# Kernel tuning notes

Measured on AMD Instinct MI355X. Metric: run time of the kernel, lower is better.

## Reference

```python
import jax, jax.numpy as jnp
from jax import lax
import numpy as np

ALIGN = 6                 # AlignW: pad width up to a multiple of align_width=6
W_BITS = 5
A_BITS = 5
A_MASK = (1 << A_BITS) - 1  # direct_conv2d bit-packs activations: keep low A_bits
DN = ('NCHW', 'OIHW', 'NCHW')


def _align_w(a):
    pad = (-a.shape[-1]) % ALIGN
    if pad:
        a = jnp.pad(a, ((0, 0), (0, 0), (0, 0), (0, pad)))
    return a


def _conv_relu(a, w, b):
    # nn.Conv2d(kernel_size=3, padding=2) + ReLU
    y = lax.conv_general_dilated(a, w, (1, 1), [(2, 2), (2, 2)], dimension_numbers=DN)
    return jax.nn.relu(y + b[None, :, None, None])


def _dc_conv(a, w):
    # DC_layer: integer direct conv2d, W_bits-quantized weights, A_bits activations,
    # stride 1, no padding (valid).
    aq = jnp.bitwise_and(a, A_MASK)
    return lax.conv_general_dilated(aq, w, (1, 1), [(0, 0), (0, 0)], dimension_numbers=DN,
                                    preferred_element_type=jnp.int32)


def _maxpool2(a):
    if jnp.issubdtype(a.dtype, jnp.floating):
        init = np.float32(-np.inf)
    else:
        init = np.int32(np.iinfo(np.int32).min)
    return lax.reduce_window(a, init, lax.max, (1, 1, 2, 2), (1, 1, 2, 2), 'VALID')


def _forward(x, ws, bs, qs, fc_w, fc_b):
    a = x
    k = 0
    for n in (2, 2, 3):          # float VGG blocks: [64,64,M, 128,128,M, 256,256,256,M]
        for _ in range(n):
            a = _conv_relu(_align_w(a), ws[k], bs[k])
            k += 1
        a = _maxpool2(a)
    # dequant stub is identity; x.int() truncates toward zero (a >= 0 after ReLU)
    xi = lax.stop_gradient(a).astype(jnp.int32)
    k = 0
    for n in (3, 3):             # DC blocks: [512,512,512,M, 512,512,512,M]
        for _ in range(n):
            xi = _dc_conv(_align_w(xi), qs[k])
            k += 1
        xi = _maxpool2(xi)
    # classifier: AdaptiveAvgPool2d((1,1)) + Flatten + Linear(512, 1000)
    pooled = jnp.mean(xi.astype(jnp.float32), axis=(2, 3))
    return pooled @ fc_w.T + fc_b


def setup_inputs() -> dict:
    key = jax.random.key(0)
    ks = jax.random.split(key, 24)
    d = {}
    d['x'] = jax.random.uniform(ks[0], (16, 3, 224, 224), jnp.float32) * 8.0
    conv_cfg = [(3, 64), (64, 64), (64, 128), (128, 128), (128, 256), (256, 256), (256, 256)]
    for i, (ci, co) in enumerate(conv_cfg):
        d[f'w{i + 1}'] = jax.random.normal(ks[1 + i], (co, ci, 3, 3), jnp.float32) * 0.1
        d[f'b{i + 1}'] = jax.random.normal(ks[8 + i], (co,), jnp.float32) * 0.1
    dc_cfg = [(256, 512)] + [(512, 512)] * 5
    for i, (ci, co) in enumerate(dc_cfg):
        # torch.randint(0, 2**W_bits - 1, ...) -> values in [0, 2**W_bits - 2]
        d[f'q{i + 1}'] = jax.random.randint(ks[15 + i], (co, ci, 3, 3), 0, 2 ** W_BITS - 1, jnp.int32)
    d['fc_w'] = jax.random.normal(ks[21], (1000, 512), jnp.float32) * 0.02
    d['fc_b'] = jnp.zeros((1000,), jnp.float32)
    return d


def reference(x, w1, w2, w3, w4, w5, w6, w7,
              b1, b2, b3, b4, b5, b6, b7,
              q1, q2, q3, q4, q5, q6, fc_w, fc_b):
    ws = (w1, w2, w3, w4, w5, w6, w7)
    bs = (b1, b2, b3, b4, b5, b6, b7)
    qs = (q1, q2, q3, q4, q5, q6)
    return _forward(x, ws, bs, qs, fc_w, fc_b)
```

## Files before the change

kernel.cpp:

```cpp
#include <hip/hip_runtime.h>
#include <cstddef>


typedef float v2f __attribute__((ext_vector_type(2)));

static __device__ __forceinline__ int dot4(int a, int b, int c) {
#if __has_builtin(__builtin_amdgcn_sdot4)
    return __builtin_amdgcn_sdot4(a, b, c, false);
#else
    return c + (a & 255) * (b & 255)
             + ((a >> 8) & 255) * ((b >> 8) & 255)
             + ((a >> 16) & 255) * ((b >> 16) & 255)
             + ((a >> 24) & 255) * ((b >> 24) & 255);
#endif
}

struct Rw { v2f a0, a1, a2, b0, b1; };

static __device__ __forceinline__ Rw ldr(const float* __restrict__ p) {
    Rw r;
    const float4 x = *reinterpret_cast<const float4*>(p);
    const float2 y = *reinterpret_cast<const float2*>(p + 4);
    const float4 z = *reinterpret_cast<const float4*>(p + 1);
    r.a0 = v2f{x.x, x.y}; r.a1 = v2f{x.z, x.w}; r.a2 = v2f{y.x, y.y};
    r.b0 = v2f{z.x, z.y}; r.b1 = v2f{z.z, z.w};
    return r;
}

static __device__ __forceinline__ void ld6i(const int* __restrict__ p, int v[6]) {
    const int4 a = *reinterpret_cast<const int4*>(p);
    const int2 b = *reinterpret_cast<const int2*>(p + 4);
    v[0] = a.x; v[1] = a.y; v[2] = a.z; v[3] = a.w; v[4] = b.x; v[5] = b.y;
}

static __device__ __forceinline__ void fmac8(const Rw v[3],
                                             const v2f* __restrict__ wr2,
                                             v2f acc[8][2])
{
#pragma unroll
    for (int kh = 0; kh < 3; ++kh) {
        const Rw r = v[kh];
#pragma unroll
        for (int c = 0; c < 8; ++c) {
            const v2f k0p = wr2[c * 9 + kh * 3 + 0];
            const v2f k1p = wr2[c * 9 + kh * 3 + 1];
            const v2f k2p = wr2[c * 9 + kh * 3 + 2];
            v2f a0 = acc[c][0];
            a0 = __builtin_elementwise_fma(r.a1, k2p, a0);
            a0 = __builtin_elementwise_fma(r.b0, k1p, a0);
            a0 = __builtin_elementwise_fma(r.a0, k0p, a0);
            acc[c][0] = a0;
            v2f a1 = acc[c][1];
            a1 = __builtin_elementwise_fma(r.a2, k2p, a1);
            a1 = __builtin_elementwise_fma(r.b1, k1p, a1);
            a1 = __builtin_elementwise_fma(r.a1, k0p, a1);
            acc[c][1] = a1;
        }
    }
}

static __device__ __forceinline__ void fmac4p(const Rw v[4],
                                              const v2f* __restrict__ wr2,
                                              v2f acc[4][2][2])
{
#pragma unroll
    for (int r = 0; r < 2; ++r) {
#pragma unroll
        for (int kh = 0; kh < 3; ++kh) {
            const Rw rv = v[r + kh];
#pragma unroll
            for (int c = 0; c < 4; ++c) {
                const v2f k0p = wr2[c * 9 + kh * 3 + 0];
                const v2f k1p = wr2[c * 9 + kh * 3 + 1];
                const v2f k2p = wr2[c * 9 + kh * 3 + 2];
                v2f a0 = acc[c][r][0];
                a0 = __builtin_elementwise_fma(rv.a1, k2p, a0);
                a0 = __builtin_elementwise_fma(rv.b0, k1p, a0);
                a0 = __builtin_elementwise_fma(rv.a0, k0p, a0);
                acc[c][r][0] = a0;
                v2f a1 = acc[c][r][1];
                a1 = __builtin_elementwise_fma(rv.a2, k2p, a1);
                a1 = __builtin_elementwise_fma(rv.b1, k1p, a1);
                a1 = __builtin_elementwise_fma(rv.a1, k0p, a1);
                acc[c][r][1] = a1;
            }
        }
    }
}

static __device__ __forceinline__ void dotc8(const int v[3][6],
                                             const int* __restrict__ wr,
                                             int acc[8][4])
{
#pragma unroll
    for (int kh = 0; kh < 3; ++kh) {
#pragma unroll
        for (int c = 0; c < 8; ++c) {
            const int k0 = wr[c * 9 + kh * 3 + 0];
            const int k1 = wr[c * 9 + kh * 3 + 1];
            const int k2 = wr[c * 9 + kh * 3 + 2];
#pragma unroll
            for (int t = 0; t < 4; ++t)
                acc[c][t] = dot4(v[kh][t], k0,
                            dot4(v[kh][t + 1], k1,
                            dot4(v[kh][t + 2], k2, acc[c][t])));
        }
    }
}

template<int CIN,int PH,int PW,int OH,int OW,int OPW,bool BORDER>
__global__ __launch_bounds__(256) void convf_k(
    const float* __restrict__ in, int instr,
    const float* __restrict__ wfp, const float* __restrict__ bias,
    float* __restrict__ out, int outstr, int total)
{
    constexpr int WB  = (OW + 3) / 4;
    constexpr int OPH = BORDER ? OH + 4 : OH;
    constexpr int OPL = OPH * OPW;
    const int s = blockIdx.z * 256 + threadIdx.x;
    if (s >= total) return;
    const int wb = s % WB;
    const int h  = (s / WB) % OH;
    const int n  = s / (WB * OH);
    const int w0 = wb * 4;
    const int cob = blockIdx.x;
    const int co0 = cob * 8;

    const float* ip = in + (size_t)n * instr + (size_t)h * PW + w0;
    const v2f* wl2 = (const v2f*)wfp + (size_t)cob * CIN * 72;

    v2f acc[8][2];
#pragma unroll
    for (int c = 0; c < 8; ++c) { acc[c][0] = (v2f)0.f; acc[c][1] = (v2f)0.f; }

    if constexpr ((CIN & 1) == 0) {
        Rw vb[3], vn[3];
#pragma unroll
        for (int kh = 0; kh < 3; ++kh) vb[kh] = ldr(ip + kh * PW);
        for (int ci = 0; ci < CIN; ci += 2) {
            ip += PH * PW;
#pragma unroll
            for (int kh = 0; kh < 3; ++kh) vn[kh] = ldr(ip + kh * PW);
            fmac8(vb, wl2 + (size_t)ci * 72, acc);
            ip += PH * PW;
#pragma unroll
            for (int kh = 0; kh < 3; ++kh) vb[kh] = ldr(ip + kh * PW);
            fmac8(vn, wl2 + (size_t)(ci + 1) * 72, acc);
        }
    } else {
#pragma unroll 1
        for (int ci = 0; ci < CIN; ++ci) {
            Rw v[3];
#pragma unroll
            for (int kh = 0; kh < 3; ++kh) v[kh] = ldr(ip + kh * PW);
            fmac8(v, wl2 + (size_t)ci * 72, acc);
            ip += PH * PW;
        }
    }

    float* ob = out + (size_t)n * outstr;
    const int ph  = BORDER ? h + 2 : h;
    const int pwo = BORDER ? 2 : 0;
#pragma unroll
    for (int c = 0; c < 8; ++c) {
        float* plane = ob + (size_t)(co0 + c) * OPL;
        float* row = plane + (size_t)ph * OPW;
        const float b = bias[co0 + c];
        const float av[4] = {acc[c][0][0], acc[c][0][1], acc[c][1][0], acc[c][1][1]};
#pragma unroll
        for (int t = 0; t < 4; ++t)
            if (w0 + t < OW) { const float r = av[t] + b; row[pwo + w0 + t] = r > 0.f ? r : 0.f; }
        if (BORDER) {
            if (wb == 0) { row[0] = 0.f; row[1] = 0.f; }
            if (wb == WB - 1) { for (int pw = OW + 2; pw < OPW; ++pw) row[pw] = 0.f; }
            if (h == 0 || h == OH - 1) {
                float* r0 = plane + (h == 0 ? 0 : (size_t)(OH + 2) * OPW);
                for (int rr = 0; rr < 2; ++rr) {
                    float* br = r0 + (size_t)rr * OPW;
#pragma unroll
                    for (int t = 0; t < 4; ++t) if (w0 + t < OW) br[2 + w0 + t] = 0.f;
                    if (wb == 0) { br[0] = 0.f; br[1] = 0.f; }
                    if (wb == WB - 1) { for (int pw = OW + 2; pw < OPW; ++pw) br[pw] = 0.f; }
                }
            }
        }
    }
}

template<int CIN,int PH,int PW,int POH,int POW,int OPW,int OY,int OX,int MODE>
__global__ __launch_bounds__(256) void convfp_k(
    const float* __restrict__ in, int instr,
    const float* __restrict__ wfp, const float* __restrict__ bias,
    void* __restrict__ outv, int outstr, int total)
{
    constexpr int WBp = POW / 2;
    constexpr int OPH = POH + 2 * OY;
    constexpr int OPL = OPH * OPW;
    const int s = blockIdx.z * 256 + threadIdx.x;
    if (s >= total) return;
    const int pb = s % WBp;
    const int ph = (s / WBp) % POH;
    const int n  = s / (WBp * POH);
    const int cob = blockIdx.x;
    const int co0 = cob * 4;

    const float* ip = in + (size_t)n * instr + (size_t)(2 * ph) * PW + 4 * pb;
    const v2f* wl2 = (const v2f*)wfp + (size_t)cob * CIN * 36;

    v2f acc[4][2][2];
#pragma unroll
    for (int c = 0; c < 4; ++c)
#pragma unroll
        for (int r = 0; r < 2; ++r) { acc[c][r][0] = (v2f)0.f; acc[c][r][1] = (v2f)0.f; }

    Rw vb[4], vn[4];
#pragma unroll
    for (int r = 0; r < 4; ++r) vb[r] = ldr(ip + r * PW);

    for (int ci = 0; ci < CIN; ci += 2) {
        ip += PH * PW;
#pragma unroll
        for (int r = 0; r < 4; ++r) vn[r] = ldr(ip + r * PW);
        fmac4p(vb, wl2 + (size_t)ci * 36, acc);
        ip += PH * PW;
#pragma unroll
        for (int r = 0; r < 4; ++r) vb[r] = ldr(ip + r * PW);
        fmac4p(vn, wl2 + (size_t)(ci + 1) * 36, acc);
    }

    float p[4][2];
#pragma unroll
    for (int c = 0; c < 4; ++c) {
        const float b = bias[co0 + c];
        float r00 = acc[c][0][0][0] + b; r00 = r00 > 0.f ? r00 : 0.f;
        float r01 = acc[c][0][0][1] + b; r01 = r01 > 0.f ? r01 : 0.f;
        float r02 = acc[c][0][1][0] + b; r02 = r02 > 0.f ? r02 : 0.f;
        float r03 = acc[c][0][1][1] + b; r03 = r03 > 0.f ? r03 : 0.f;
        float r10 = acc[c][1][0][0] + b; r10 = r10 > 0.f ? r10 : 0.f;
        float r11 = acc[c][1][0][1] + b; r11 = r11 > 0.f ? r11 : 0.f;
        float r12 = acc[c][1][1][0] + b; r12 = r12 > 0.f ? r12 : 0.f;
        float r13 = acc[c][1][1][1] + b; r13 = r13 > 0.f ? r13 : 0.f;
        float p0 = r00; p0 = p0 > r01 ? p0 : r01; p0 = p0 > r10 ? p0 : r10; p0 = p0 > r11 ? p0 : r11;
        float p1 = r02; p1 = p1 > r03 ? p1 : r03; p1 = p1 > r12 ? p1 : r12; p1 = p1 > r13 ? p1 : r13;
        p[c][0] = p0; p[c][1] = p1;
    }

    if constexpr (MODE == 1) {
        int* base = (int*)outv + (size_t)n * outstr + (size_t)cob * OPL
                  + (size_t)(OY + ph) * OPW + OX + 2 * pb;
        base[0] = (((int)p[0][0]) & 31) | ((((int)p[1][0]) & 31) << 8)
                | ((((int)p[2][0]) & 31) << 16) | ((((int)p[3][0]) & 31) << 24);
        base[1] = (((int)p[0][1]) & 31) | ((((int)p[1][1]) & 31) << 8)
                | ((((int)p[2][1]) & 31) << 16) | ((((int)p[3][1]) & 31) << 24);
        if (pb == WBp - 1) {
            int* row = (int*)outv + (size_t)n * outstr + (size_t)cob * OPL
                     + (size_t)(OY + ph) * OPW;
            for (int pw = OX + POW; pw < OPW; ++pw) row[pw] = 0;
        }
    } else {
#pragma unroll
        for (int c = 0; c < 4; ++c) {
            float* plane = (float*)outv + (size_t)n * outstr + (size_t)(co0 + c) * OPL;
            float* row = plane + (size_t)(OY + ph) * OPW;
            row[OX + 2 * pb]     = p[c][0];
            row[OX + 2 * pb + 1] = p[c][1];
            if (OX > 0 && pb == 0) { row[0] = 0.f; row[1] = 0.f; }
            if (pb == WBp - 1) { for (int pw = OX + POW; pw < OPW; ++pw) row[pw] = 0.f; }
            if (OY > 0 && (ph == 0 || ph == POH - 1)) {
                float* r0 = plane + (ph == 0 ? 0 : (size_t)(OY + POH) * OPW);
                for (int rr = 0; rr < OY; ++rr) {
                    float* br = r0 + (size_t)rr * OPW;
                    br[OX + 2 * pb] = 0.f; br[OX + 2 * pb + 1] = 0.f;
                    if (pb == 0) { br[0] = 0.f; br[1] = 0.f; }
                    if (pb == WBp - 1) { for (int pw = OX + POW; pw < OPW; ++pw) br[pw] = 0.f; }
                }
            }
        }
    }
}

template<int CIN4,int PH,int PW,int OH,int OW,int OPW,bool PACKOUT>
__global__ __launch_bounds__(256) void convq_k(
    const int* __restrict__ in, int instr, const int* __restrict__ wqp,
    int* __restrict__ out, int outstr, int total)
{
    constexpr int WB  = (OW + 3) / 4;
    constexpr int OPL = OH * OPW;
    const int s = blockIdx.z * 256 + threadIdx.x;
    if (s >= total) return;
    const int wb = s % WB;
    const int h  = (s / WB) % OH;
    const int n  = s / (WB * OH);
    const int w0 = wb * 4;
    const int cob = blockIdx.x;
    const int co0 = cob * 8;

    const int* ip = in + (size_t)n * instr + (size_t)h * PW + w0;
    const int* wl = wqp + (size_t)cob * CIN4 * 72;

    int acc[8][4];
#pragma unroll
    for (int c = 0; c < 8; ++c)
#pragma unroll
        for (int t = 0; t < 4; ++t) acc[c][t] = 0;

    int vb[3][6], vn[3][6];
#pragma unroll
    for (int kh = 0; kh < 3; ++kh) ld6i(ip + kh * PW, vb[kh]);

    for (int ci = 0; ci < CIN4; ci += 2) {
        ip += PH * PW;
#pragma unroll
        for (int kh = 0; kh < 3; ++kh) ld6i(ip + kh * PW, vn[kh]);
        dotc8(vb, wl + (size_t)ci * 72, acc);
        ip += PH * PW;
#pragma unroll
        for (int kh = 0; kh < 3; ++kh) ld6i(ip + kh * PW, vb[kh]);
        dotc8(vn, wl + (size_t)(ci + 1) * 72, acc);
    }

    if (PACKOUT) {
        int* base = out + (size_t)n * outstr + (size_t)(cob * 2) * OPL + (size_t)h * OPW + w0;
#pragma unroll
        for (int t = 0; t < 4; ++t) {
            if (w0 + t < OW) {
                const int lo = (acc[0][t] & 31) | ((acc[1][t] & 31) << 8)
                             | ((acc[2][t] & 31) << 16) | ((acc[3][t] & 31) << 24);
                const int hi = (acc[4][t] & 31) | ((acc[5][t] & 31) << 8)
                             | ((acc[6][t] & 31) << 16) | ((acc[7][t] & 31) << 24);
                base[t] = lo;
                base[OPL + t] = hi;
            }
        }
        if (wb == WB - 1) {
            for (int pw = OW; pw < OPW; ++pw) { base[pw - w0] = 0; base[OPL + pw - w0] = 0; }
        }
    } else {
        int* ob = out + (size_t)n * outstr;
#pragma unroll
        for (int c = 0; c < 8; ++c) {
            int* row = ob + (size_t)(co0 + c) * OPL + (size_t)h * OPW;
#pragma unroll
            for (int t = 0; t < 4; ++t)
                if (w0 + t < OW) row[w0 + t] = acc[c][t];
            if (wb == WB - 1) { for (int pw = OW; pw < OPW; ++pw) row[pw] = 0; }
        }
    }
}

__global__ void pack_wf_k(const float* __restrict__ w, float* __restrict__ out,
                          int CIN, int TC, int total)
{
    const int i = blockIdx.x * 256 + threadIdx.x;
    if (i >= total) return;
    const int r = i % 9;
    const int c = (i / 9) % TC;
    const int t = i / (9 * TC);
    const int ci = t % CIN;
    const int cob = t / CIN;
    const float v = w[(((size_t)cob * TC + c) * CIN + ci) * 9 + r];
    out[2 * i]     = v;
    out[2 * i + 1] = v;
}

__global__ void pack_wq_k(const int* __restrict__ q, int* __restrict__ out,
                          int CIN4, int total)
{
    const int i = blockIdx.x * 256 + threadIdx.x;
    if (i >= total) return;
    const int r = i % 9;
    const int c = (i / 9) % 8;
    const int t = i / 72;
    const int ci4 = t % CIN4;
    const int cob = t / CIN4;
    const int co = cob * 8 + c;
    const int* p = q + ((size_t)co * CIN4 * 4 + ci4 * 4) * 9 + r;
    out[i] = (p[0] & 255) | ((p[9] & 255) << 8) | ((p[18] & 255) << 16) | ((p[27] & 255) << 24);
}

template<int C4,int HI,int WI,int HO,int WO,int OPH,int OPW>
__global__ void poolpack_k(const int* __restrict__ in, int instr,
                           int* __restrict__ out, int outstr, int total)
{
    const int i = blockIdx.x * 256 + threadIdx.x;
    if (i >= total) return;
    int t = i;
    const int px = t % OPW; t /= OPW;
    const int py = t % OPH; t /= OPH;
    const int c4 = t % C4;  const int n = t / C4;
    int word = 0;
    if (py < HO && px < WO) {
#pragma unroll
        for (int j = 0; j < 4; ++j) {
            const int* p = in + (size_t)n * instr
                         + ((size_t)(c4 * 4 + j) * HI + 2 * py) * WI + 2 * px;
            int m = p[0];
            m = m > p[1] ? m : p[1];
            m = m > p[WI] ? m : p[WI];
            m = m > p[WI + 1] ? m : p[WI + 1];
            word |= (m & 31) << (8 * j);
        }
    }
    out[(size_t)n * outstr + ((size_t)c4 * OPH + py) * OPW + px] = word;
}

template<int C,int HI,int WI,int HO,int WO,int OPH,int OPW>
__global__ void pool_i_k(const int* __restrict__ in, int instr,
                         int* __restrict__ out, int outstr, int total)
{
    const int i = blockIdx.x * 256 + threadIdx.x;
    if (i >= total) return;
    constexpr int OPL = OPH * OPW;
    int t = i;
    const int px = t % OPW; t /= OPW;
    const int py = t % OPH; t /= OPH;
    const int c  = t % C;   const int n = t / C;
    int v = 0;
    if (py < HO && px < WO) {
        const int* p = in + (size_t)n * instr + ((size_t)c * HI + 2 * py) * WI + 2 * px;
        int m = p[0];
        m = m > p[1] ? m : p[1];
        m = m > p[WI] ? m : p[WI];
        m = m > p[WI + 1] ? m : p[WI + 1];
        v = m;
    }
    out[(size_t)n * outstr + (size_t)c * OPL + (size_t)py * OPW + px] = v;
}

__global__ void copyin_k(const float* __restrict__ x, float* __restrict__ dst,
                         int outstr, int total)
{
    const int i = blockIdx.x * 256 + threadIdx.x;
    if (i >= total) return;
    int t = i;
    const int pw = t % 232; t /= 232;
    const int ph = t % 228; t /= 228;
    const int c  = t % 3;   const int n = t / 3;
    float v = 0.f;
    const int y = ph - 2, xx = pw - 2;
    if ((unsigned)y < 224u && (unsigned)xx < 224u)
        v = x[(size_t)n * 150528 + ((size_t)c * 224 + y) * 224 + xx];
    dst[(size_t)n * outstr + ((size_t)c * 228 + ph) * 232 + pw] = v;
}

__global__ void pool_mean_k(const int* __restrict__ in, int instr,
                            float* __restrict__ out, int outstr, int total)
{
    const int i = blockIdx.x * 256 + threadIdx.x;
    if (i >= total) return;
    const int n = i / 512, c = i % 512;
    const int* p = in + (size_t)n * instr + (size_t)c * 33;
    int s = 0;
#pragma unroll
    for (int j = 0; j < 33; ++j) s += p[j];
    out[(size_t)n * outstr + c] = (float)s / 33.0f;
}

__global__ void fc_k(const float* __restrict__ pooled, const float* __restrict__ w,
                     const float* __restrict__ b, float* __restrict__ out,
                     int nb, int n0)
{
    const int i = blockIdx.x * 256 + threadIdx.x;
    if (i >= nb * 1000) return;
    const int co = i % 1000;
    const int n  = i / 1000;
    const float4* pv = (const float4*)(pooled + (size_t)n * 512);
    const float4* wr = (const float4*)(w + (size_t)co * 512);
    float s = b[co];
    for (int c = 0; c < 128; ++c) {
        const float4 a = pv[c], q = wr[c];
        s = fmaf(a.x, q.x, s); s = fmaf(a.y, q.y, s);
        s = fmaf(a.z, q.z, s); s = fmaf(a.w, q.w, s);
    }
    out[(size_t)(n0 + n) * 1000 + co] = s;
}

extern "C" void kernel_launch(void* const* d_in, const int* in_sizes, int n_in,
                              void* d_out, int out_size, void* d_ws, size_t ws_size,
                              hipStream_t stream)
{
    (void)n_in; (void)out_size;
    const float* x = (const float*)d_in[0];
    const float* W[7]; const float* Bv[7]; const int* Q[6];
    const bool inter = (in_sizes[2] == 64);
    for (int i = 0; i < 7; ++i) {
        if (inter) { W[i] = (const float*)d_in[1 + 2 * i]; Bv[i] = (const float*)d_in[2 + 2 * i]; }
        else       { W[i] = (const float*)d_in[1 + i];     Bv[i] = (const float*)d_in[8 + i];     }
    }
    for (int i = 0; i < 6; ++i) Q[i] = (const int*)d_in[15 + i];
    const float* fcw = (const float*)d_in[21];
    const float* fcb = (const float*)d_in[22];
    float* outp = (float*)d_out;

    static const int FCO[7]  = {64, 64, 128, 128, 256, 256, 256};
    static const int FCIN[7] = {3, 64, 64, 128, 128, 256, 256};
    static const int FTC[7]  = {8, 4, 8, 4, 8, 8, 4};
    static const int QCIN4[6] = {64, 128, 128, 128, 128, 128};
    size_t wfoff[7], wft = 0;
    for (int i = 0; i < 7; ++i) { wfoff[i] = wft; wft += (size_t)FCO[i] * FCIN[i] * 9 * 2; }
    size_t wqoff[6], wqt = 0;
    for (int i = 0; i < 6; ++i) { wqoff[i] = wqt; wqt += (size_t)512 * QCIN4[i] * 9 * 4; }
    const size_t WTOT = wft + wqt;

    float* wfb = (float*)d_ws;
    int*   wqb = (int*)((float*)d_ws + wft);
    for (int i = 0; i < 7; ++i) {
        const int total = FCO[i] * FCIN[i] * 9;
        pack_wf_k<<<(total + 255) / 256, 256, 0, stream>>>(W[i], wfb + wfoff[i], FCIN[i], FTC[i], total);
    }
    for (int i = 0; i < 6; ++i) {
        const int total = 512 * QCIN4[i] * 9;
        pack_wq_k<<<(total + 255) / 256, 256, 0, stream>>>(Q[i], wqb + wqoff[i], QCIN4[i], total);
    }

    const long long SZ_X0 = 158688,  SZ_F1 = 3532800, SZ_P1 = 936448;
    const long long SZ_F4 = 2027520, SZ_P2 = 580608,  SZ_F7 = 1264640;
    const long long SZ_F8 = 1440768, SZ_PK1 = 90112;
    const long long SZ_D1 = 168960,  SZ_D2 = 157696,  SZ_D3 = 532480;
    const long long SZ_PK4 = 39936,  SZ_D4 = 33792,   SZ_D5 = 27648;
    const long long SZ_D6 = 86016,   SZ_P5 = 16896;
    const long long DCH = SZ_D1 + SZ_D2 + SZ_D3 + SZ_PK4 + SZ_D4 + SZ_D5 + SZ_D6 + SZ_P5 + 512;

    float* AR = (float*)d_ws + WTOT;
    long long AE2 = ((long long)(ws_size / 4) - (long long)WTOT - 65536) & ~3LL;

    int nbB = 16;
    for (;; nbB >>= 1) {
        if (nbB == 1) break;
        const long long f = nbB;
        const long long low = (nbB == 16) ? 0 : SZ_P1 * 16;
        const bool ok = (SZ_P1 * 16 + SZ_F4 * f <= AE2)
                     && (low + SZ_P2 * f <= AE2 - SZ_F4 * f)
                     && (low + SZ_F8 * f <= AE2 - SZ_F7 * f)
                     && (low + SZ_F8 * f <= AE2 - SZ_PK1 * f)
                     && (low + DCH * f <= AE2 - SZ_PK1 * f);
        if (ok) break;
    }
    int cA = 16;
    while (cA > 1 && SZ_P1 * 16 + (SZ_X0 + SZ_F1) * cA > AE2) cA >>= 1;

    const long long lowb = (nbB == 16) ? 0 : SZ_P1 * 16;
    float* tP1 = AR;
    float* tX0 = AR + SZ_P1 * 16;
    float* tF1 = tX0 + SZ_X0 * cA;
    float* tF4 = AR + (AE2 - SZ_F4 * nbB);
    float* tP2 = AR + lowb;
    float* tF7 = AR + (AE2 - SZ_F7 * nbB);
    float* tF8 = AR + lowb;
    int*   tPK1 = (int*)(AR + (AE2 - SZ_PK1 * nbB));
    int*   tD1 = (int*)(AR + lowb);
    int*   tD2 = tD1 + SZ_D1 * nbB;
    int*   tD3 = tD2 + SZ_D2 * nbB;
    int*   tPK4 = tD3 + SZ_D3 * nbB;
    int*   tD4 = tPK4 + SZ_PK4 * nbB;
    int*   tD5 = tD4 + SZ_D4 * nbB;
    int*   tD6 = tD5 + SZ_D5 * nbB;
    int*   tP5 = tD6 + SZ_D6 * nbB;
    float* tPP = (float*)(tP5 + SZ_P5 * nbB);

    for (int a0 = 0; a0 < 16; a0 += cA) {
        const int nb = cA;
        {
            const int total = nb * 3 * 228 * 232;
            copyin_k<<<(total + 255) / 256, 256, 0, stream>>>(
                x + (size_t)a0 * 150528, tX0, (int)SZ_X0, total);
        }
        {
            const int total = nb * 226 * 58;
            dim3 g(8, 1, (total + 255) / 256);
            convf_k<3, 228, 232, 226, 230, 240, true><<<g, 256, 0, stream>>>(
                tX0, (int)SZ_X0, wfb + wfoff[0], Bv[0], tF1, (int)SZ_F1, total);
        }
        {
            const int total = nb * 114 * 59;
            dim3 g(16, 1, (total + 255) / 256);
            convfp_k<64, 230, 240, 114, 118, 124, 2, 2, 0><<<g, 256, 0, stream>>>(
                tF1, (int)SZ_F1, wfb + wfoff[1], Bv[1],
                tP1 + (size_t)a0 * SZ_P1, (int)SZ_P1, total);
        }
    }

    for (int b0 = 0; b0 < 16; b0 += nbB) {
        const int nb = nbB;
        {
            const int total = nb * 116 * 31;
            dim3 g(16, 1, (total + 255) / 256);
            convf_k<64, 118, 124, 116, 122, 132, true><<<g, 256, 0, stream>>>(
                tP1 + (size_t)b0 * SZ_P1, (int)SZ_P1, wfb + wfoff[2], Bv[2],
                tF4, (int)SZ_F4, total);
        }
        {
            const int total = nb * 59 * 32;
            dim3 g(32, 1, (total + 255) / 256);
            convfp_k<128, 120, 132, 59, 64, 72, 2, 2, 0><<<g, 256, 0, stream>>>(
                tF4, (int)SZ_F4, wfb + wfoff[3], Bv[3], tP2, (int)SZ_P2, total);
        }
        {
            const int total = nb * 61 * 17;
            dim3 g(32, 1, (total + 255) / 256);
            convf_k<128, 63, 72, 61, 68, 76, true><<<g, 256, 0, stream>>>(
                tP2, (int)SZ_P2, wfb + wfoff[4], Bv[4], tF7, (int)SZ_F7, total);
        }
        {
            const int total = nb * 63 * 19;
            dim3 g(32, 1, (total + 255) / 256);
            convf_k<256, 65, 76, 63, 74, 84, true><<<g, 256, 0, stream>>>(
                tF7, (int)SZ_F7, wfb + wfoff[5], Bv[5], tF8, (int)SZ_F8, total);
        }
        {
            const int total = nb * 32 * 20;
            dim3 g(64, 1, (total + 255) / 256);
            convfp_k<256, 67, 84, 32, 40, 44, 0, 0, 1><<<g, 256, 0, stream>>>(
                tF8, (int)SZ_F8, wfb + wfoff[6], Bv[6], (void*)tPK1, (int)SZ_PK1, total);
        }
        {
            const int total = nb * 30 * 10;
            dim3 g(64, 1, (total + 255) / 256);
            convq_k<64, 32, 44, 30, 40, 44, true><<<g, 256, 0, stream>>>(
                tPK1, (int)SZ_PK1, wqb + wqoff[0], tD1, (int)SZ_D1, total);
        }
        {
            const int total = nb * 28 * 10;
            dim3 g(64, 1, (total + 255) / 256);
            convq_k<128, 30, 44, 28, 40, 44, true><<<g, 256, 0, stream>>>(
                tD1, (int)SZ_D1, wqb + wqoff[1], tD2, (int)SZ_D2, total);
        }
        {
            const int total = nb * 26 * 10;
            dim3 g(64, 1, (total + 255) / 256);
            convq_k<128, 28, 44, 26, 40, 40, false><<<g, 256, 0, stream>>>(
                tD2, (int)SZ_D2, wqb + wqoff[2], tD3, (int)SZ_D3, total);
        }
        {
            const int total = nb * 128 * 13 * 24;
            poolpack_k<128, 26, 40, 13, 20, 13, 24><<<(total + 255) / 256, 256, 0, stream>>>(
                tD3, (int)SZ_D3, tPK4, (int)SZ_PK4, total);
        }
        {
            const int total = nb * 11 * 6;
            dim3 g(64, 1, (total + 255) / 256);
            convq_k<128, 13, 24, 11, 22, 24, true><<<g, 256, 0, stream>>>(
                tPK4, (int)SZ_PK4, wqb + wqoff[3], tD4, (int)SZ_D4, total);
        }
        {
            const int total = nb * 9 * 6;
            dim3 g(64, 1, (total + 255) / 256);
            convq_k<128, 11, 24, 9, 22, 24, true><<<g, 256, 0, stream>>>(
                tD4, (int)SZ_D4, wqb + wqoff[4], tD5, (int)SZ_D5, total);
        }
        {
            const int total = nb * 7 * 6;
            dim3 g(64, 1, (total + 255) / 256);
            convq_k<128, 9, 24, 7, 22, 24, false><<<g, 256, 0, stream>>>(
                tD5, (int)SZ_D5, wqb + wqoff[5], tD6, (int)SZ_D6, total);
        }
        {
            const int total = nb * 512 * 33;
            pool_i_k<512, 7, 24, 3, 11, 3, 11><<<(total + 255) / 256, 256, 0, stream>>>(
                tD6, (int)SZ_D6, tP5, (int)SZ_P5, total);
        }
        {
            const int total = nb * 512;
            pool_mean_k<<<(total + 255) / 256, 256, 0, stream>>>(
                tP5, (int)SZ_P5, tPP, 512, total);
        }
        {
            const int total = nb * 1000;
            fc_k<<<(total + 255) / 256, 256, 0, stream>>>(tPP, fcw, fcb, outp, nb, b0);
        }
    }
}
```

Measured before the change: 5.810 ms.

## Stage conv weights in shared memory per input-channel chunk

Each block now copies a chunk of packed weights (32 or 64 input channels) into LDS with a cooperative float4/int4 load, then reads the weights from LDS in the inner FMA/dot4 loops instead of reading them from global memory in each thread. Out-of-range threads no longer return early, so they can take part in the barriers; they clamp their index and skip the stores. The aim is to cut redundant global and scalar-cache weight traffic, at the cost of two barriers per chunk and LDS reads. LDS reads may be slower than the uniform scalar loads the compiler could emit before, and the added LDS use may lower occupancy.

```diff
diff --git a/kernel.cpp b/kernel.cpp
--- a/kernel.cpp
+++ b/kernel.cpp
@@ -33,8 +33,7 @@
     v[0] = a.x; v[1] = a.y; v[2] = a.z; v[3] = a.w; v[4] = b.x; v[5] = b.y;
 }
 
-static __device__ __forceinline__ void fmac8(const Rw v[3],
-                                             const v2f* __restrict__ wr2,
+static __device__ __forceinline__ void fmac8(const Rw v[3], const v2f* wr2,
                                              v2f acc[8][2])
 {
 #pragma unroll
@@ -59,8 +58,7 @@
     }
 }
 
-static __device__ __forceinline__ void fmac4p(const Rw v[4],
-                                              const v2f* __restrict__ wr2,
+static __device__ __forceinline__ void fmac4p(const Rw v[4], const v2f* wr2,
                                               v2f acc[4][2][2])
 {
 #pragma unroll
@@ -88,8 +86,7 @@
     }
 }
 
-static __device__ __forceinline__ void dotc8(const int v[3][6],
-                                             const int* __restrict__ wr,
+static __device__ __forceinline__ void dotc8(const int v[3][6], const int* wr,
                                              int acc[8][4])
 {
 #pragma unroll
@@ -117,8 +114,9 @@
     constexpr int WB  = (OW + 3) / 4;
     constexpr int OPH = BORDER ? OH + 4 : OH;
     constexpr int OPL = OPH * OPW;
-    const int s = blockIdx.z * 256 + threadIdx.x;
-    if (s >= total) return;
+    const int sraw = blockIdx.z * 256 + threadIdx.x;
+    const bool act = sraw < total;
+    const int s = act ? sraw : total - 1;
     const int wb = s % WB;
     const int h  = (s / WB) % OH;
     const int n  = s / (WB * OH);
@@ -127,25 +125,35 @@
     const int co0 = cob * 8;
 
     const float* ip = in + (size_t)n * instr + (size_t)h * PW + w0;
-    const v2f* wl2 = (const v2f*)wfp + (size_t)cob * CIN * 72;
+    const float* wlf = wfp + (size_t)cob * CIN * 144;
 
     v2f acc[8][2];
 #pragma unroll
     for (int c = 0; c < 8; ++c) { acc[c][0] = (v2f)0.f; acc[c][1] = (v2f)0.f; }
 
-    if constexpr ((CIN & 1) == 0) {
+    if constexpr ((CIN % 32) == 0) {
+        __shared__ float lw[32 * 144];
         Rw vb[3], vn[3];
 #pragma unroll
         for (int kh = 0; kh < 3; ++kh) vb[kh] = ldr(ip + kh * PW);
-        for (int ci = 0; ci < CIN; ci += 2) {
-            ip += PH * PW;
-#pragma unroll
-            for (int kh = 0; kh < 3; ++kh) vn[kh] = ldr(ip + kh * PW);
-            fmac8(vb, wl2 + (size_t)ci * 72, acc);
-            ip += PH * PW;
-#pragma unroll
-            for (int kh = 0; kh < 3; ++kh) vb[kh] = ldr(ip + kh * PW);
-            fmac8(vn, wl2 + (size_t)(ci + 1) * 72, acc);
+        for (int base = 0; base < CIN; base += 32) {
+            __syncthreads();
+            {
+                const float4* src = (const float4*)(wlf + (size_t)base * 144);
+                float4* dst = (float4*)lw;
+                for (int i = threadIdx.x; i < 1152; i += 256) dst[i] = src[i];
+            }
+            __syncthreads();
+            for (int u = 0; u < 32; u += 2) {
+                ip += PH * PW;
+#pragma unroll
+                for (int kh = 0; kh < 3; ++kh) vn[kh] = ldr(ip + kh * PW);
+                fmac8(vb, (const v2f*)(lw + u * 144), acc);
+                ip += PH * PW;
+#pragma unroll
+                for (int kh = 0; kh < 3; ++kh) vb[kh] = ldr(ip + kh * PW);
+                fmac8(vn, (const v2f*)(lw + (u + 1) * 144), acc);
+            }
         }
     } else {
 #pragma unroll 1
@@ -153,34 +161,36 @@
             Rw v[3];
 #pragma unroll
             for (int kh = 0; kh < 3; ++kh) v[kh] = ldr(ip + kh * PW);
-            fmac8(v, wl2 + (size_t)ci * 72, acc);
+            fmac8(v, (const v2f*)(wlf + (size_t)ci * 144), acc);
             ip += PH * PW;
         }
     }
 
-    float* ob = out + (size_t)n * outstr;
-    const int ph  = BORDER ? h + 2 : h;
-    const int pwo = BORDER ? 2 : 0;
-#pragma unroll
-    for (int c = 0; c < 8; ++c) {
-        float* plane = ob + (size_t)(co0 + c) * OPL;
-        float* row = plane + (size_t)ph * OPW;
-        const float b = bias[co0 + c];
-        const float av[4] = {acc[c][0][0], acc[c][0][1], acc[c][1][0], acc[c][1][1]};
-#pragma unroll
-        for (int t = 0; t < 4; ++t)
-            if (w0 + t < OW) { const float r = av[t] + b; row[pwo + w0 + t] = r > 0.f ? r : 0.f; }
-        if (BORDER) {
-            if (wb == 0) { row[0] = 0.f; row[1] = 0.f; }
-            if (wb == WB - 1) { for (int pw = OW + 2; pw < OPW; ++pw) row[pw] = 0.f; }
-            if (h == 0 || h == OH - 1) {
-                float* r0 = plane + (h == 0 ? 0 : (size_t)(OH + 2) * OPW);
-                for (int rr = 0; rr < 2; ++rr) {
-                    float* br = r0 + (size_t)rr * OPW;
-#pragma unroll
-                    for (int t = 0; t < 4; ++t) if (w0 + t < OW) br[2 + w0 + t] = 0.f;
-                    if (wb == 0) { br[0] = 0.f; br[1] = 0.f; }
-                    if (wb == WB - 1) { for (int pw = OW + 2; pw < OPW; ++pw) br[pw] = 0.f; }
+    if (act) {
+        float* ob = out + (size_t)n * outstr;
+        const int ph  = BORDER ? h + 2 : h;
+        const int pwo = BORDER ? 2 : 0;
+#pragma unroll
+        for (int c = 0; c < 8; ++c) {
+            float* plane = ob + (size_t)(co0 + c) * OPL;
+            float* row = plane + (size_t)ph * OPW;
+            const float b = bias[co0 + c];
+            const float av[4] = {acc[c][0][0], acc[c][0][1], acc[c][1][0], acc[c][1][1]};
+#pragma unroll
+            for (int t = 0; t < 4; ++t)
+                if (w0 + t < OW) { const float r = av[t] + b; row[pwo + w0 + t] = r > 0.f ? r : 0.f; }
+            if (BORDER) {
+                if (wb == 0) { row[0] = 0.f; row[1] = 0.f; }
+                if (wb == WB - 1) { for (int pw = OW + 2; pw < OPW; ++pw) row[pw] = 0.f; }
+                if (h == 0 || h == OH - 1) {
+                    float* r0 = plane + (h == 0 ? 0 : (size_t)(OH + 2) * OPW);
+                    for (int rr = 0; rr < 2; ++rr) {
+                        float* br = r0 + (size_t)rr * OPW;
+#pragma unroll
+                        for (int t = 0; t < 4; ++t) if (w0 + t < OW) br[2 + w0 + t] = 0.f;
+                        if (wb == 0) { br[0] = 0.f; br[1] = 0.f; }
+                        if (wb == WB - 1) { for (int pw = OW + 2; pw < OPW; ++pw) br[pw] = 0.f; }
+                    }
                 }
             }
         }
@@ -196,8 +206,9 @@
     constexpr int WBp = POW / 2;
     constexpr int OPH = POH + 2 * OY;
     constexpr int OPL = OPH * OPW;
-    const int s = blockIdx.z * 256 + threadIdx.x;
-    if (s >= total) return;
+    const int sraw = blockIdx.z * 256 + threadIdx.x;
+    const bool act = sraw < total;
+    const int s = act ? sraw : total - 1;
     const int pb = s % WBp;
     const int ph = (s / WBp) % POH;
     const int n  = s / (WBp * POH);
@@ -205,7 +216,7 @@
     const int co0 = cob * 4;
 
     const float* ip = in + (size_t)n * instr + (size_t)(2 * ph) * PW + 4 * pb;
-    const v2f* wl2 = (const v2f*)wfp + (size_t)cob * CIN * 36;
+    const float* wlf = wfp + (size_t)cob * CIN * 72;
 
     v2f acc[4][2][2];
 #pragma unroll
@@ -213,66 +224,78 @@
 #pragma unroll
         for (int r = 0; r < 2; ++r) { acc[c][r][0] = (v2f)0.f; acc[c][r][1] = (v2f)0.f; }
 
+    __shared__ float lw[64 * 72];
     Rw vb[4], vn[4];
 #pragma unroll
     for (int r = 0; r < 4; ++r) vb[r] = ldr(ip + r * PW);
 
-    for (int ci = 0; ci < CIN; ci += 2) {
-        ip += PH * PW;
-#pragma unroll
-        for (int r = 0; r < 4; ++r) vn[r] = ldr(ip + r * PW);
-        fmac4p(vb, wl2 + (size_t)ci * 36, acc);
-        ip += PH * PW;
-#pragma unroll
-        for (int r = 0; r < 4; ++r) vb[r] = ldr(ip + r * PW);
-        fmac4p(vn, wl2 + (size_t)(ci + 1) * 36, acc);
-    }
-
-    float p[4][2];
-#pragma unroll
-    for (int c = 0; c < 4; ++c) {
-        const float b = bias[co0 + c];
-        float r00 = acc[c][0][0][0] + b; r00 = r00 > 0.f ? r00 : 0.f;
-        float r01 = acc[c][0][0][1] + b; r01 = r01 > 0.f ? r01 : 0.f;
-        float r02 = acc[c][0][1][0] + b; r02 = r02 > 0.f ? r02 : 0.f;
-        float r03 = acc[c][0][1][1] + b; r03 = r03 > 0.f ? r03 : 0.f;
-        float r10 = acc[c][1][0][0] + b; r10 = r10 > 0.f ? r10 : 0.f;
-        float r11 = acc[c][1][0][1] + b; r11 = r11 > 0.f ? r11 : 0.f;
-        float r12 = acc[c][1][1][0] + b; r12 = r12 > 0.f ? r12 : 0.f;
-        float r13 = acc[c][1][1][1] + b; r13 = r13 > 0.f ? r13 : 0.f;
-        float p0 = r00; p0 = p0 > r01 ? p0 : r01; p0 = p0 > r10 ? p0 : r10; p0 = p0 > r11 ? p0 : r11;
-        float p1 = r02; p1 = p1 > r03 ? p1 : r03; p1 = p1 > r12 ? p1 : r12; p1 = p1 > r13 ? p1 : r13;
-        p[c][0] = p0; p[c][1] = p1;
-    }
-
-    if constexpr (MODE == 1) {
-        int* base = (int*)outv + (size_t)n * outstr + (size_t)cob * OPL
-                  + (size_t)(OY + ph) * OPW + OX + 2 * pb;
-        base[0] = (((int)p[0][0]) & 31) | ((((int)p[1][0]) & 31) << 8)
-                | ((((int)p[2][0]) & 31) << 16) | ((((int)p[3][0]) & 31) << 24);
-        base[1] = (((int)p[0][1]) & 31) | ((((int)p[1][1]) & 31) << 8)
-                | ((((int)p[2][1]) & 31) << 16) | ((((int)p[3][1]) & 31) << 24);
-        if (pb == WBp - 1) {
-            int* row = (int*)outv + (size_t)n * outstr + (size_t)cob * OPL
-                     + (size_t)(OY + ph) * OPW;
-            for (int pw = OX + POW; pw < OPW; ++pw) row[pw] = 0;
-        }
-    } else {
+    for (int base = 0; base < CIN; base += 64) {
+        __syncthreads();
+        {
+            const float4* src = (const float4*)(wlf + (size_t)base * 72);
+            float4* dst = (float4*)lw;
+            for (int i = threadIdx.x; i < 1152; i += 256) dst[i] = src[i];
+        }
+        __syncthreads();
+        for (int u = 0; u < 64; u += 2) {
+            ip += PH * PW;
+#pragma unroll
+            for (int r = 0; r < 4; ++r) vn[r] = ldr(ip + r * PW);
+            fmac4p(vb, (const v2f*)(lw + u * 72), acc);
+            ip += PH * PW;
+#pragma unroll
+            for (int r = 0; r < 4; ++r) vb[r] = ldr(ip + r * PW);
+            fmac4p(vn, (const v2f*)(lw + (u + 1) * 72), acc);
+        }
+    }
+
+    if (act) {
+        float p[4][2];
 #pragma unroll
         for (int c = 0; c < 4; ++c) {
-            float* plane = (float*)outv + (size_t)n * outstr + (size_t)(co0 + c) * OPL;
-            float* row = plane + (size_t)(OY + ph) * OPW;
-            row[OX + 2 * pb]     = p[c][0];
-            row[OX + 2 * pb + 1] = p[c][1];
-            if (OX > 0 && pb == 0) { row[0] = 0.f; row[1] = 0.f; }
-            if (pb == WBp - 1) { for (int pw = OX + POW; pw < OPW; ++pw) row[pw] = 0.f; }
-            if (OY > 0 && (ph == 0 || ph == POH - 1)) {
-                float* r0 = plane + (ph == 0 ? 0 : (size_t)(OY + POH) * OPW);
-                for (int rr = 0; rr < OY; ++rr) {
-                    float* br = r0 + (size_t)rr * OPW;
-                    br[OX + 2 * pb] = 0.f; br[OX + 2 * pb + 1] = 0.f;
-                    if (pb == 0) { br[0] = 0.f; br[1] = 0.f; }
-                    if (pb == WBp - 1) { for (int pw = OX + POW; pw < OPW; ++pw) br[pw] = 0.f; }
+            const float b = bias[co0 + c];
+            float r00 = acc[c][0][0][0] + b; r00 = r00 > 0.f ? r00 : 0.f;
+            float r01 = acc[c][0][0][1] + b; r01 = r01 > 0.f ? r01 : 0.f;
+            float r02 = acc[c][0][1][0] + b; r02 = r02 > 0.f ? r02 : 0.f;
+            float r03 = acc[c][0][1][1] + b; r03 = r03 > 0.f ? r03 : 0.f;
+            float r10 = acc[c][1][0][0] + b; r10 = r10 > 0.f ? r10 : 0.f;
+            float r11 = acc[c][1][0][1] + b; r11 = r11 > 0.f ? r11 : 0.f;
+            float r12 = acc[c][1][1][0] + b; r12 = r12 > 0.f ? r12 : 0.f;
+            float r13 = acc[c][1][1][1] + b; r13 = r13 > 0.f ? r13 : 0.f;
+            float p0 = r00; p0 = p0 > r01 ? p0 : r01; p0 = p0 > r10 ? p0 : r10; p0 = p0 > r11 ? p0 : r11;
+            float p1 = r02; p1 = p1 > r03 ? p1 : r03; p1 = p1 > r12 ? p1 : r12; p1 = p1 > r13 ? p1 : r13;
+            p[c][0] = p0; p[c][1] = p1;
+        }
+
+        if constexpr (MODE == 1) {
+            int* base2 = (int*)outv + (size_t)n * outstr + (size_t)cob * OPL
+                       + (size_t)(OY + ph) * OPW + OX + 2 * pb;
+            base2[0] = (((int)p[0][0]) & 31) | ((((int)p[1][0]) & 31) << 8)
+                     | ((((int)p[2][0]) & 31) << 16) | ((((int)p[3][0]) & 31) << 24);
+            base2[1] = (((int)p[0][1]) & 31) | ((((int)p[1][1]) & 31) << 8)
+                     | ((((int)p[2][1]) & 31) << 16) | ((((int)p[3][1]) & 31) << 24);
+            if (pb == WBp - 1) {
+                int* row = (int*)outv + (size_t)n * outstr + (size_t)cob * OPL
+                         + (size_t)(OY + ph) * OPW;
+                for (int pw = OX + POW; pw < OPW; ++pw) row[pw] = 0;
+            }
+        } else {
+#pragma unroll
+            for (int c = 0; c < 4; ++c) {
+                float* plane = (float*)outv + (size_t)n * outstr + (size_t)(co0 + c) * OPL;
+                float* row = plane + (size_t)(OY + ph) * OPW;
+                row[OX + 2 * pb]     = p[c][0];
+                row[OX + 2 * pb + 1] = p[c][1];
+                if (OX > 0 && pb == 0) { row[0] = 0.f; row[1] = 0.f; }
+                if (pb == WBp - 1) { for (int pw = OX + POW; pw < OPW; ++pw) row[pw] = 0.f; }
+                if (OY > 0 && (ph == 0 || ph == POH - 1)) {
+                    float* r0 = plane + (ph == 0 ? 0 : (size_t)(OY + POH) * OPW);
+                    for (int rr = 0; rr < OY; ++rr) {
+                        float* br = r0 + (size_t)rr * OPW;
+                        br[OX + 2 * pb] = 0.f; br[OX + 2 * pb + 1] = 0.f;
+                        if (pb == 0) { br[0] = 0.f; br[1] = 0.f; }
+                        if (pb == WBp - 1) { for (int pw = OX + POW; pw < OPW; ++pw) br[pw] = 0.f; }
+                    }
                 }
             }
         }
@@ -286,8 +309,9 @@
 {
     constexpr int WB  = (OW + 3) / 4;
     constexpr int OPL = OH * OPW;
-    const int s = blockIdx.z * 256 + threadIdx.x;
-    if (s >= total) return;
+    const int sraw = blockIdx.z * 256 + threadIdx.x;
+    const bool act = sraw < total;
+    const int s = act ? sraw : total - 1;
     const int wb = s % WB;
     const int h  = (s / WB) % OH;
     const int n  = s / (WB * OH);
@@ -304,46 +328,58 @@
 #pragma unroll
         for (int t = 0; t < 4; ++t) acc[c][t] = 0;
 
+    __shared__ int lwq[64 * 72];
     int vb[3][6], vn[3][6];
 #pragma unroll
     for (int kh = 0; kh < 3; ++kh) ld6i(ip + kh * PW, vb[kh]);
 
-    for (int ci = 0; ci < CIN4; ci += 2) {
-        ip += PH * PW;
-#pragma unroll
-        for (int kh = 0; kh < 3; ++kh) ld6i(ip + kh * PW, vn[kh]);
-        dotc8(vb, wl + (size_t)ci * 72, acc);
-        ip += PH * PW;
-#pragma unroll
-        for (int kh = 0; kh < 3; ++kh) ld6i(ip + kh * PW, vb[kh]);
-        dotc8(vn, wl + (size_t)(ci + 1) * 72, acc);
-    }
-
-    if (PACKOUT) {
-        int* base = out + (size_t)n * outstr + (size_t)(cob * 2) * OPL + (size_t)h * OPW + w0;
-#pragma unroll
-        for (int t = 0; t < 4; ++t) {
-            if (w0 + t < OW) {
-                const int lo = (acc[0][t] & 31) | ((acc[1][t] & 31) << 8)
-                             | ((acc[2][t] & 31) << 16) | ((acc[3][t] & 31) << 24);
-                const int hi = (acc[4][t] & 31) | ((acc[5][t] & 31) << 8)
-                             | ((acc[6][t] & 31) << 16) | ((acc[7][t] & 31) << 24);
-                base[t] = lo;
-                base[OPL + t] = hi;
-            }
-        }
-        if (wb == WB - 1) {
-            for (int pw = OW; pw < OPW; ++pw) { base[pw - w0] = 0; base[OPL + pw - w0] = 0; }
-        }
-    } else {
-        int* ob = out + (size_t)n * outstr;
-#pragma unroll
-        for (int c = 0; c < 8; ++c) {
-            int* row = ob + (size_t)(co0 + c) * OPL + (size_t)h * OPW;
-#pragma unroll
-            for (int t = 0; t < 4; ++t)
-                if (w0 + t < OW) row[w0 + t] = acc[c][t];
-            if (wb == WB - 1) { for (int pw = OW; pw < OPW; ++pw) row[pw] = 0; }
+    for (int base = 0; base < CIN4; base += 64) {
+        __syncthreads();
+        {
+            const int4* src = (const int4*)(wl + (size_t)base * 72);
+            int4* dst = (int4*)lwq;
+            for (int i = threadIdx.x; i < 1152; i += 256) dst[i] = src[i];
+        }
+        __syncthreads();
+        for (int u = 0; u < 64; u += 2) {
+            ip += PH * PW;
+#pragma unroll
+            for (int kh = 0; kh < 3; ++kh) ld6i(ip + kh * PW, vn[kh]);
+            dotc8(vb, lwq + u * 72, acc);
+            ip += PH * PW;
+#pragma unroll
+            for (int kh = 0; kh < 3; ++kh) ld6i(ip + kh * PW, vb[kh]);
+            dotc8(vn, lwq + (u + 1) * 72, acc);
+        }
+    }
+
+    if (act) {
+        if (PACKOUT) {
+            int* base2 = out + (size_t)n * outstr + (size_t)(cob * 2) * OPL + (size_t)h * OPW + w0;
+#pragma unroll
+            for (int t = 0; t < 4; ++t) {
+                if (w0 + t < OW) {
+                    const int lo = (acc[0][t] & 31) | ((acc[1][t] & 31) << 8)
+                                 | ((acc[2][t] & 31) << 16) | ((acc[3][t] & 31) << 24);
+                    const int hi = (acc[4][t] & 31) | ((acc[5][t] & 31) << 8)
+                                 | ((acc[6][t] & 31) << 16) | ((acc[7][t] & 31) << 24);
+                    base2[t] = lo;
+                    base2[OPL + t] = hi;
+                }
+            }
+            if (wb == WB - 1) {
+                for (int pw = OW; pw < OPW; ++pw) { base2[pw - w0] = 0; base2[OPL + pw - w0] = 0; }
+            }
+        } else {
+            int* ob = out + (size_t)n * outstr;
+#pragma unroll
+            for (int c = 0; c < 8; ++c) {
+                int* row = ob + (size_t)(co0 + c) * OPL + (size_t)h * OPW;
+#pragma unroll
+                for (int t = 0; t < 4; ++t)
+                    if (w0 + t < OW) row[w0 + t] = acc[c][t];
+                if (wb == WB - 1) { for (int pw = OW; pw < OPW; ++pw) row[pw] = 0; }
+            }
         }
     }
 }
```

Result: slower. 6.253 ms (+7.6%).
